# Kernel optimization log

Hardware: AMD Instinct MI355X
Metric: run time of the kernel (lower is better)

The kernel has to match this reference:

```python
import jax, jax.numpy as jnp
import numpy as np

LN_EPS = 1e-5


def setup_inputs() -> dict:
    key = jax.random.key(0)
    ks = jax.random.split(key, 3)
    B, C, H, W = 2, 256, 64, 64
    x = jax.random.normal(ks[0], (B, C, H, W), dtype=jnp.float32)
    ln_gamma = jnp.ones((C,), dtype=jnp.float32)
    ln_beta = jnp.zeros((C,), dtype=jnp.float32)
    w_qkv = jax.random.normal(ks[1], (3 * C, C), dtype=jnp.float32) * 0.02
    w_proj = jax.random.normal(ks[2], (C, C), dtype=jnp.float32) * 0.02
    b_proj = jnp.zeros((C,), dtype=jnp.float32)
    return {"x": x, "ln_gamma": ln_gamma, "ln_beta": ln_beta,
            "w_qkv": w_qkv, "w_proj": w_proj, "b_proj": b_proj}


def reference(x, ln_gamma, ln_beta, w_qkv, w_proj, b_proj):
    B, C, H, W = x.shape
    num_heads = 8
    head_dim = C // num_heads
    scale = head_dim ** -0.5

    # patch2token: B C H W -> B N C
    t = x.reshape(B, C, H * W).transpose(0, 2, 1)
    res = t

    # LayerNorm over channel dim
    mu = t.mean(-1, keepdims=True)
    var = t.var(-1, keepdims=True)
    tn = (t - mu) * jax.lax.rsqrt(var + LN_EPS) * ln_gamma + ln_beta

    # qkv projection (torch Linear: y = x @ W.T)
    N = H * W
    qkv = jnp.einsum('bnc,oc->bno', tn, w_qkv)  # B N 3C
    qkv = qkv.reshape(B, N, 3, num_heads, head_dim).transpose(2, 0, 3, 1, 4)
    q, k, v = qkv[0], qkv[1], qkv[2]  # each B h N d

    attn = jnp.einsum('bhnd,bhmd->bhnm', q, k) * scale  # B h N N
    attn = jax.nn.softmax(attn, axis=-1)
    out = jnp.einsum('bhnm,bhmd->bhnd', attn, v)  # B h N d
    out = out.transpose(0, 2, 1, 3).reshape(B, N, C)

    out = jnp.einsum('bnc,oc->bno', out, w_proj) + b_proj
    out = res + out

    # token2patch: B N C -> B C H W
    return out.transpose(0, 2, 1).reshape(B, C, H, W)
```

## Files before the change

### kernel.cpp

```cpp
#include <hip/hip_runtime.h>

typedef __bf16 bf16x8 __attribute__((ext_vector_type(8)));
typedef float f32x16 __attribute__((ext_vector_type(16)));
typedef unsigned int uint4v __attribute__((ext_vector_type(4)));
typedef unsigned int uint2v __attribute__((ext_vector_type(2)));
typedef unsigned short u16;

#define MFMA32(a, b, c) __builtin_amdgcn_mfma_f32_32x32x16_bf16((a), (b), (c), 0, 0, 0)

static __device__ __forceinline__ u16 f2bf(float f) {
  unsigned u = __builtin_bit_cast(unsigned, f);
  u += 0x7fffu + ((u >> 16) & 1u);
  return (u16)(u >> 16);
}

static __device__ __forceinline__ f32x16 zero16() {
  f32x16 z;
#pragma unroll
  for (int i = 0; i < 16; ++i) z[i] = 0.0f;
  return z;
}


__global__ __launch_bounds__(256) void prep_kernel(
    const float* __restrict__ x, const float* __restrict__ gamma,
    const float* __restrict__ beta, const float* __restrict__ wq,
    const float* __restrict__ wp, u16* __restrict__ tnf,
    u16* __restrict__ wqf, u16* __restrict__ wpf) {
  int bid = blockIdx.x;
  int t = threadIdx.x;
  if (bid >= 256) {
    int u = ((bid - 256) << 2) + (t >> 6);
    int l = t & 63, lo = l & 31, hi = l >> 5;
    const float* src; u16* dst; int ot, s;
    if (u < 384) { ot = u >> 4; s = u & 15; src = wq; dst = wqf; }
    else { int u2 = u - 384; ot = u2 >> 4; s = u2 & 15; src = wp; dst = wpf; }
    const float* p = src + (ot * 32 + lo) * 256 + s * 16 + 8 * hi;
    bf16x8 f;
#pragma unroll
    for (int i = 0; i < 8; ++i) f[i] = (__bf16)p[i];
    *(bf16x8*)(dst + (ot * 16 + s) * 512 + l * 8) = f;
    return;
  }
  __shared__ float xs[32][257];
  __shared__ float red[2][8][32];
  __shared__ float mu_s[32], rs_s[32];
  __shared__ float gs[256], bs[256];
  int ni = t & 31, g = t >> 5;
  int mt = bid;
  int n0 = mt * 32;
  int b = n0 >> 12, nn = n0 & 4095;
  gs[t] = gamma[t]; bs[t] = beta[t];
  float s1 = 0.f, s2 = 0.f;
  for (int c = g; c < 256; c += 8) {
    float v = x[(((b << 8) + c) << 12) + nn + ni];
    xs[ni][c] = v;
    s1 += v; s2 += v * v;
  }
  red[0][g][ni] = s1; red[1][g][ni] = s2;
  __syncthreads();
  if (t < 32) {
    float ss = 0.f, qq = 0.f;
#pragma unroll
    for (int k = 0; k < 8; ++k) { ss += red[0][k][t]; qq += red[1][k][t]; }
    float mean = ss * (1.f / 256.f);
    float var = qq * (1.f / 256.f) - mean * mean;
    mu_s[t] = mean;
    rs_s[t] = rsqrtf(var + 1e-5f);
  }
  __syncthreads();
  int l = t & 63, w = t >> 6, lo = l & 31, hi = l >> 5;
  float mu = mu_s[lo], rs = rs_s[lo];
#pragma unroll
  for (int jj = 0; jj < 4; ++jj) {
    int s = w * 4 + jj;
    bf16x8 f;
#pragma unroll
    for (int i = 0; i < 8; ++i) {
      int c = s * 16 + 8 * hi + i;
      f[i] = (__bf16)((xs[lo][c] - mu) * rs * gs[c] + bs[c]);
    }
    *(bf16x8*)(tnf + (mt * 16 + s) * 512 + l * 8) = f;
  }
}

__global__ __launch_bounds__(64) void qkv_gemm(
    const u16* __restrict__ tnf, const u16* __restrict__ wqf,
    u16* __restrict__ qg, u16* __restrict__ kf, u16* __restrict__ vf) {
  __shared__ u16 ls[32][32];
  int l = threadIdx.x, lo = l & 31, hi = l >> 5;
  int ot = blockIdx.x % 24, mt = blockIdx.x / 24;
  int m0 = mt * 32, o0 = ot * 32;
  f32x16 acc = zero16();
  const bf16x8* ap = (const bf16x8*)(tnf + (mt * 16) * 512 + l * 8);
  const bf16x8* bp = (const bf16x8*)(wqf + (ot * 16) * 512 + l * 8);
#pragma unroll
  for (int s = 0; s < 16; ++s) acc = MFMA32(ap[s * 64], bp[s * 64], acc);
  int sec = o0 >> 8;
  int hh = (o0 & 255) >> 5;
  const float sl2e = 0.17677669529663688f * 1.4426950408889634f;
  float mul = (sec == 0) ? sl2e : 1.0f;
  if (sec == 2) {
#pragma unroll
    for (int r = 0; r < 16; ++r) {
      int row = (r & 3) + 8 * (r >> 2) + 4 * hi;
      ls[lo][row] = f2bf(acc[r]);
    }
  } else {
#pragma unroll
    for (int r = 0; r < 16; ++r) {
      int row = (r & 3) + 8 * (r >> 2) + 4 * hi;
      ls[row][lo] = f2bf(acc[r] * mul);
    }
  }
  __syncthreads();
  int b = m0 >> 12, n0 = m0 & 4095;
  int bh = (b << 3) + hh;
  if (sec == 0) {
    u16* dst = qg + (((bh << 12) + n0 + (l >> 1)) << 5) + (l & 1) * 16;
    const u16* srow = &ls[l >> 1][(l & 1) * 16];
    *(uint4v*)(dst) = *(const uint4v*)(srow);
    *(uint4v*)(dst + 8) = *(const uint4v*)(srow + 8);
  } else {
    u16* base = (sec == 1) ? kf : vf;
    int tt = n0 >> 5;
    u16* dst = base + ((bh * 128 + tt) * 2) * 512 + l * 8;
    *(uint4v*)(dst) = *(const uint4v*)&ls[lo][8 * hi];
    *(uint4v*)(dst + 512) = *(const uint4v*)&ls[lo][16 + 8 * hi];
  }
}

__global__ __launch_bounds__(512) void attn_proj_kernel(
    const u16* __restrict__ qg, const u16* __restrict__ kf,
    const u16* __restrict__ vf, const u16* __restrict__ wpf,
    const float* __restrict__ bpj, const float* __restrict__ x,
    float* __restrict__ out) {
  __shared__ u16 ls_all[8][32][32];
  __shared__ float lsf[8][32][33];
  int t = threadIdx.x;
  int l = t & 63, w = t >> 6, lo = l & 31, hi = l >> 5;
  int b = blockIdx.x >> 7, qt = blockIdx.x & 127;
  int bh = (b << 3) + w;
  const u16* qp = qg + (((bh << 12) + qt * 32 + lo) << 5);
  bf16x8 qf0 = *(const bf16x8*)(qp + hi * 8);
  bf16x8 qf1 = *(const bf16x8*)(qp + 16 + hi * 8);
  const u16* kfb = kf + (size_t)bh * 131072 + l * 8;
  const u16* vfb = vf + (size_t)bh * 131072 + l * 8;
  const f32x16 zf = zero16();
  f32x16 oacc = zero16();
  f32x16 lacc = zero16();
  const uint4v onesu = {0x3F803F80u, 0x3F803F80u, 0x3F803F80u, 0x3F803F80u};
  const bf16x8 ones8 = __builtin_bit_cast(bf16x8, onesu);

#define LOADT(T, K0, K1, V0, V1) do {                  \
    const u16* kq_ = kfb + (T) * 1024;                 \
    const u16* vq_ = vfb + (T) * 1024;                 \
    K0 = *(const bf16x8*)(kq_);                        \
    K1 = *(const bf16x8*)(kq_ + 512);                  \
    V0 = *(const bf16x8*)(vq_);                        \
    V1 = *(const bf16x8*)(vq_ + 512);                  \
  } while (0)

#define ABODY(K0, K1, V0, V1) do {                                          \
    f32x16 sa = MFMA32(K0, qf0, zf);                                        \
    sa = MFMA32(K1, qf1, sa);                                               \
    f32x16 tmag = sa * 128.0f + 8404864.0f;                                 \
    unsigned pk[8];                                                         \
    _Pragma("unroll")                                                       \
    for (int j = 0; j < 8; ++j) {                                           \
      pk[j] = __builtin_amdgcn_perm(                                        \
          __builtin_bit_cast(unsigned, tmag[2 * j + 1]),                    \
          __builtin_bit_cast(unsigned, tmag[2 * j]), 0x05040100u);          \
    }                                                                       \
    uint2v A0 = __builtin_amdgcn_permlane32_swap(pk[0], pk[2], false, false); \
    uint2v A1 = __builtin_amdgcn_permlane32_swap(pk[1], pk[3], false, false); \
    uint2v B0 = __builtin_amdgcn_permlane32_swap(pk[4], pk[6], false, false); \
    uint2v B1 = __builtin_amdgcn_permlane32_swap(pk[5], pk[7], false, false); \
    uint4v u0v = {A0[0], A1[0], A0[1], A1[1]};                              \
    uint4v u1v = {B0[0], B1[0], B0[1], B1[1]};                              \
    bf16x8 p0 = __builtin_bit_cast(bf16x8, u0v);                            \
    bf16x8 p1 = __builtin_bit_cast(bf16x8, u1v);                            \
    __builtin_amdgcn_s_setprio(1);                                          \
    oacc = MFMA32(V0, p0, oacc);                                            \
    lacc = MFMA32(ones8, p0, lacc);                                         \
    oacc = MFMA32(V1, p1, oacc);                                            \
    lacc = MFMA32(ones8, p1, lacc);                                         \
    __builtin_amdgcn_s_setprio(0);                                          \
  } while (0)

  bf16x8 ak0, ak1, av0, av1, bk0, bk1, bv0, bv1;
  LOADT(0, ak0, ak1, av0, av1);
  LOADT(1, bk0, bk1, bv0, bv1);
  for (int tt = 0; tt < 128; tt += 2) {
    bf16x8 ck0, ck1, cv0, cv1, dk0, dk1, dv0, dv1;
    if (tt + 2 < 128) LOADT(tt + 2, ck0, ck1, cv0, cv1);
    ABODY(ak0, ak1, av0, av1);
    if (tt + 3 < 128) LOADT(tt + 3, dk0, dk1, dv0, dv1);
    ABODY(bk0, bk1, bv0, bv1);
    ak0 = ck0; ak1 = ck1; av0 = cv0; av1 = cv1;
    bk0 = dk0; bk1 = dk1; bv0 = dv0; bv1 = dv1;
  }
#undef LOADT
#undef ABODY

  float inv = 1.0f / lacc[0];
#pragma unroll
  for (int r = 0; r < 16; ++r) {
    int row = (r & 3) + 8 * (r >> 2) + 4 * hi;
    ls_all[w][lo][row] = f2bf(oacc[r] * inv);
  }
  __syncthreads();

  f32x16 acc = zero16();
  const bf16x8* bp = (const bf16x8*)(wpf + (w * 16) * 512 + l * 8);
#pragma unroll
  for (int s = 0; s < 16; ++s) {
    bf16x8 af = *(const bf16x8*)&ls_all[s >> 1][lo][(s & 1) * 16 + 8 * hi];
    acc = MFMA32(af, bp[s * 64], acc);
  }
  int c0 = w * 32;
  float bias = bpj[c0 + lo];
#pragma unroll
  for (int r = 0; r < 16; ++r) {
    int row = (r & 3) + 8 * (r >> 2) + 4 * hi;
    lsf[w][row][lo] = acc[r] + bias;
  }
  int n0 = qt * 32;
#pragma unroll
  for (int r2 = 0; r2 < 16; ++r2) {
    int cl = 2 * r2 + hi;
    int idx = (((b << 8) + c0 + cl) << 12) + n0 + lo;
    out[idx] = lsf[w][lo][cl] + x[idx];
  }
}

extern "C" void kernel_launch(void* const* d_in, const int* in_sizes, int n_in,
                              void* d_out, int out_size, void* d_ws, size_t ws_size,
                              hipStream_t stream) {
  const float* x      = (const float*)d_in[0];
  const float* gamma  = (const float*)d_in[1];
  const float* beta   = (const float*)d_in[2];
  const float* w_qkv  = (const float*)d_in[3];
  const float* w_proj = (const float*)d_in[4];
  const float* b_proj = (const float*)d_in[5];
  float* out = (float*)d_out;
  char* ws = (char*)d_ws;
  const size_t MB = 1024 * 1024;
  u16* tnf = (u16*)(ws);
  u16* qg  = (u16*)(ws + 4 * MB);
  u16* kf  = (u16*)(ws + 8 * MB);
  u16* vf  = (u16*)(ws + 12 * MB);
  u16* wqf = (u16*)(ws + 16 * MB);
  u16* wpf = (u16*)(ws + 16 * MB + 768 * 256 * sizeof(u16));

  hipLaunchKernelGGL(prep_kernel, dim3(384), dim3(256), 0, stream,
                     x, gamma, beta, w_qkv, w_proj, tnf, wqf, wpf);
  hipLaunchKernelGGL(qkv_gemm, dim3(6144), dim3(64), 0, stream,
                     tnf, wqf, qg, kf, vf);
  hipLaunchKernelGGL(attn_proj_kernel, dim3(256), dim3(512), 0, stream,
                     qg, kf, vf, wpf, b_proj, x, out);
}
```

Measured before the change: 136.0 us.

## Fuse LayerNorm with QKV GEMM, keeping normalized tokens in shared memory

Weight conversion is split into its own small kernel. LayerNorm is merged with the QKV projection: each block normalizes 32 tokens into shared memory, and its 4 waves each compute 6 output tiles from register-held A fragments. This drops the global round trip of the normalized activations and the 6144-block GEMM launch. In exchange only 256 blocks do the GEMM work, so parallelism is lower, and each block reads all the weights.

```diff
diff --git a/kernel.cpp b/kernel.cpp
--- a/kernel.cpp
+++ b/kernel.cpp
@@ -22,34 +22,37 @@
 }
 
 
-__global__ __launch_bounds__(256) void prep_kernel(
+__global__ __launch_bounds__(256) void convw_kernel(
+    const float* __restrict__ wq, const float* __restrict__ wp,
+    u16* __restrict__ wqf, u16* __restrict__ wpf) {
+  int t = threadIdx.x;
+  int u = (blockIdx.x << 2) + (t >> 6);
+  int l = t & 63, lo = l & 31, hi = l >> 5;
+  const float* src; u16* dst; int ot, s;
+  if (u < 384) { ot = u >> 4; s = u & 15; src = wq; dst = wqf; }
+  else { int u2 = u - 384; ot = u2 >> 4; s = u2 & 15; src = wp; dst = wpf; }
+  const float* p = src + (ot * 32 + lo) * 256 + s * 16 + 8 * hi;
+  bf16x8 f;
+#pragma unroll
+  for (int i = 0; i < 8; ++i) f[i] = (__bf16)p[i];
+  *(bf16x8*)(dst + (ot * 16 + s) * 512 + l * 8) = f;
+}
+
+__global__ __launch_bounds__(256) void prepqkv_kernel(
     const float* __restrict__ x, const float* __restrict__ gamma,
-    const float* __restrict__ beta, const float* __restrict__ wq,
-    const float* __restrict__ wp, u16* __restrict__ tnf,
-    u16* __restrict__ wqf, u16* __restrict__ wpf) {
-  int bid = blockIdx.x;
-  int t = threadIdx.x;
-  if (bid >= 256) {
-    int u = ((bid - 256) << 2) + (t >> 6);
-    int l = t & 63, lo = l & 31, hi = l >> 5;
-    const float* src; u16* dst; int ot, s;
-    if (u < 384) { ot = u >> 4; s = u & 15; src = wq; dst = wqf; }
-    else { int u2 = u - 384; ot = u2 >> 4; s = u2 & 15; src = wp; dst = wpf; }
-    const float* p = src + (ot * 32 + lo) * 256 + s * 16 + 8 * hi;
-    bf16x8 f;
-#pragma unroll
-    for (int i = 0; i < 8; ++i) f[i] = (__bf16)p[i];
-    *(bf16x8*)(dst + (ot * 16 + s) * 512 + l * 8) = f;
-    return;
-  }
+    const float* __restrict__ beta, const u16* __restrict__ wqf,
+    u16* __restrict__ qg, u16* __restrict__ kf, u16* __restrict__ vf) {
   __shared__ float xs[32][257];
   __shared__ float red[2][8][32];
   __shared__ float mu_s[32], rs_s[32];
   __shared__ float gs[256], bs[256];
+  __shared__ u16 af[16 * 512];
+  __shared__ u16 lsb[4][32][32];
+  int t = threadIdx.x;
+  int mt = blockIdx.x;
+  int n0g = mt * 32;
+  int b = n0g >> 12, nn = n0g & 4095;
   int ni = t & 31, g = t >> 5;
-  int mt = bid;
-  int n0 = mt * 32;
-  int b = n0 >> 12, nn = n0 & 4095;
   gs[t] = gamma[t]; bs[t] = beta[t];
   float s1 = 0.f, s2 = 0.f;
   for (int c = g; c < 256; c += 8) {
@@ -70,63 +73,64 @@
   }
   __syncthreads();
   int l = t & 63, w = t >> 6, lo = l & 31, hi = l >> 5;
-  float mu = mu_s[lo], rs = rs_s[lo];
-#pragma unroll
-  for (int jj = 0; jj < 4; ++jj) {
-    int s = w * 4 + jj;
-    bf16x8 f;
-#pragma unroll
-    for (int i = 0; i < 8; ++i) {
-      int c = s * 16 + 8 * hi + i;
-      f[i] = (__bf16)((xs[lo][c] - mu) * rs * gs[c] + bs[c]);
+  {
+    float mu = mu_s[lo], rs = rs_s[lo];
+#pragma unroll
+    for (int jj = 0; jj < 4; ++jj) {
+      int s = w * 4 + jj;
+      bf16x8 f;
+#pragma unroll
+      for (int i = 0; i < 8; ++i) {
+        int c = s * 16 + 8 * hi + i;
+        f[i] = (__bf16)((xs[lo][c] - mu) * rs * gs[c] + bs[c]);
+      }
+      *(bf16x8*)(af + s * 512 + l * 8) = f;
     }
-    *(bf16x8*)(tnf + (mt * 16 + s) * 512 + l * 8) = f;
-  }
-}
-
-__global__ __launch_bounds__(64) void qkv_gemm(
-    const u16* __restrict__ tnf, const u16* __restrict__ wqf,
-    u16* __restrict__ qg, u16* __restrict__ kf, u16* __restrict__ vf) {
-  __shared__ u16 ls[32][32];
-  int l = threadIdx.x, lo = l & 31, hi = l >> 5;
-  int ot = blockIdx.x % 24, mt = blockIdx.x / 24;
-  int m0 = mt * 32, o0 = ot * 32;
-  f32x16 acc = zero16();
-  const bf16x8* ap = (const bf16x8*)(tnf + (mt * 16) * 512 + l * 8);
-  const bf16x8* bp = (const bf16x8*)(wqf + (ot * 16) * 512 + l * 8);
-#pragma unroll
-  for (int s = 0; s < 16; ++s) acc = MFMA32(ap[s * 64], bp[s * 64], acc);
-  int sec = o0 >> 8;
-  int hh = (o0 & 255) >> 5;
+  }
+  __syncthreads();
+
+  bf16x8 ar[16];
+#pragma unroll
+  for (int s = 0; s < 16; ++s) ar[s] = *(const bf16x8*)(af + s * 512 + l * 8);
   const float sl2e = 0.17677669529663688f * 1.4426950408889634f;
-  float mul = (sec == 0) ? sl2e : 1.0f;
-  if (sec == 2) {
-#pragma unroll
-    for (int r = 0; r < 16; ++r) {
-      int row = (r & 3) + 8 * (r >> 2) + 4 * hi;
-      ls[lo][row] = f2bf(acc[r]);
+  int bb = n0g >> 12, n0 = n0g & 4095;
+  int tt = n0 >> 5;
+#pragma unroll
+  for (int oi = 0; oi < 6; ++oi) {
+    int ot = w * 6 + oi;
+    int o0 = ot * 32;
+    f32x16 acc = zero16();
+    const bf16x8* bp = (const bf16x8*)(wqf + (ot * 16) * 512 + l * 8);
+#pragma unroll
+    for (int s = 0; s < 16; ++s) acc = MFMA32(ar[s], bp[s * 64], acc);
+    int sec = o0 >> 8;
+    int hh = (o0 & 255) >> 5;
+    float mul = (sec == 0) ? sl2e : 1.0f;
+    if (sec == 2) {
+#pragma unroll
+      for (int r = 0; r < 16; ++r) {
+        int row = (r & 3) + 8 * (r >> 2) + 4 * hi;
+        lsb[w][lo][row] = f2bf(acc[r]);
+      }
+    } else {
+#pragma unroll
+      for (int r = 0; r < 16; ++r) {
+        int row = (r & 3) + 8 * (r >> 2) + 4 * hi;
+        lsb[w][row][lo] = f2bf(acc[r] * mul);
+      }
     }
-  } else {
-#pragma unroll
-    for (int r = 0; r < 16; ++r) {
-      int row = (r & 3) + 8 * (r >> 2) + 4 * hi;
-      ls[row][lo] = f2bf(acc[r] * mul);
+    int bh = (bb << 3) + hh;
+    if (sec == 0) {
+      u16* dst = qg + (((bh << 12) + n0 + (l >> 1)) << 5) + (l & 1) * 16;
+      const u16* srow = &lsb[w][l >> 1][(l & 1) * 16];
+      *(uint4v*)(dst) = *(const uint4v*)(srow);
+      *(uint4v*)(dst + 8) = *(const uint4v*)(srow + 8);
+    } else {
+      u16* base = (sec == 1) ? kf : vf;
+      u16* dst = base + ((bh * 128 + tt) * 2) * 512 + l * 8;
+      *(uint4v*)(dst) = *(const uint4v*)&lsb[w][lo][8 * hi];
+      *(uint4v*)(dst + 512) = *(const uint4v*)&lsb[w][lo][16 + 8 * hi];
     }
-  }
-  __syncthreads();
-  int b = m0 >> 12, n0 = m0 & 4095;
-  int bh = (b << 3) + hh;
-  if (sec == 0) {
-    u16* dst = qg + (((bh << 12) + n0 + (l >> 1)) << 5) + (l & 1) * 16;
-    const u16* srow = &ls[l >> 1][(l & 1) * 16];
-    *(uint4v*)(dst) = *(const uint4v*)(srow);
-    *(uint4v*)(dst + 8) = *(const uint4v*)(srow + 8);
-  } else {
-    u16* base = (sec == 1) ? kf : vf;
-    int tt = n0 >> 5;
-    u16* dst = base + ((bh * 128 + tt) * 2) * 512 + l * 8;
-    *(uint4v*)(dst) = *(const uint4v*)&ls[lo][8 * hi];
-    *(uint4v*)(dst + 512) = *(const uint4v*)&ls[lo][16 + 8 * hi];
   }
 }
 
@@ -246,17 +250,16 @@
   float* out = (float*)d_out;
   char* ws = (char*)d_ws;
   const size_t MB = 1024 * 1024;
-  u16* tnf = (u16*)(ws);
-  u16* qg  = (u16*)(ws + 4 * MB);
-  u16* kf  = (u16*)(ws + 8 * MB);
-  u16* vf  = (u16*)(ws + 12 * MB);
-  u16* wqf = (u16*)(ws + 16 * MB);
-  u16* wpf = (u16*)(ws + 16 * MB + 768 * 256 * sizeof(u16));
-
-  hipLaunchKernelGGL(prep_kernel, dim3(384), dim3(256), 0, stream,
-                     x, gamma, beta, w_qkv, w_proj, tnf, wqf, wpf);
-  hipLaunchKernelGGL(qkv_gemm, dim3(6144), dim3(64), 0, stream,
-                     tnf, wqf, qg, kf, vf);
+  u16* qg  = (u16*)(ws);
+  u16* kf  = (u16*)(ws + 4 * MB);
+  u16* vf  = (u16*)(ws + 8 * MB);
+  u16* wqf = (u16*)(ws + 12 * MB);
+  u16* wpf = (u16*)(ws + 12 * MB + 768 * 256 * sizeof(u16));
+
+  hipLaunchKernelGGL(convw_kernel, dim3(128), dim3(256), 0, stream,
+                     w_qkv, w_proj, wqf, wpf);
+  hipLaunchKernelGGL(prepqkv_kernel, dim3(256), dim3(256), 0, stream,
+                     x, gamma, beta, wqf, qg, kf, vf);
   hipLaunchKernelGGL(attn_proj_kernel, dim3(256), dim3(512), 0, stream,
                      qg, kf, vf, wpf, b_proj, x, out);
 }
```

After: 141.3 us. 1.04x slower.
